# Optimization experiments

Hardware: AMD Instinct MI355X
Metric: run time of the kernel (lower is better)

## Reference

```python
import jax, jax.numpy as jnp
import numpy as np

B, N, E = 2, 2048, 1024
H, D = 16, 64


def setup_inputs() -> dict:
    key = jax.random.key(0)
    k1, k2, k3 = jax.random.split(key, 3)
    x = jax.random.normal(k1, (B, N, E), dtype=jnp.float32)
    Wqkv = jax.random.normal(k2, (3 * H * D, E), dtype=jnp.float32) * 0.02
    bqkv = jnp.zeros((3 * H * D,), dtype=jnp.float32)
    Wout = jax.random.normal(k3, (E, H * D), dtype=jnp.float32) * 0.02
    bout = jnp.zeros((E,), dtype=jnp.float32)
    return {"x": x, "Wqkv": Wqkv, "bqkv": bqkv, "Wout": Wout, "bout": bout}


def reference(x, Wqkv, bqkv, Wout, bout):
    b, n, _ = x.shape
    scale = D ** (-0.5)
    # qkv projection: [b, n, 3*h*d], interpreted as (h, d, qkv) per einops pattern
    qkv = (x @ Wqkv.T + bqkv).reshape(b, n, H, D, 3)
    q = jnp.transpose(qkv[..., 0], (0, 2, 1, 3))  # [b, h, n, d]
    k = jnp.transpose(qkv[..., 1], (0, 2, 1, 3))
    v = jnp.transpose(qkv[..., 2], (0, 2, 1, 3))
    att = jnp.einsum('bhid,bhjd->bhij', q, k) * scale  # [b, h, n, n]
    causal = jnp.tril(jnp.ones((n, n), dtype=bool))
    att = jnp.where(causal, att, -jnp.inf)
    att = jax.nn.softmax(att, axis=-1)
    out = jnp.einsum('bhij,bhjd->bhid', att, v)  # [b, h, n, d]
    out = jnp.transpose(out, (0, 2, 1, 3)).reshape(b, n, H * D)
    return out @ Wout.T + bout
```

## Files before the change

### kernel.cpp

```cpp
#include <hip/hip_runtime.h>
#include <hip/hip_bf16.h>

#define B_ 2
#define N_ 2048
#define E_ 1024
#define H_ 16
#define D_ 64
#define M_ 4096
#define HD_ 1024
#define NT_ 3072

using f32x4  = __attribute__((ext_vector_type(4))) float;
using f32x16 = __attribute__((ext_vector_type(16))) float;
using bf16x8 = __attribute__((ext_vector_type(8))) short;

static __device__ __forceinline__ unsigned short f2bf(float f) {
  union { float f; unsigned u; } v; v.f = f;
  unsigned r = v.u + 0x7FFF + ((v.u >> 16) & 1);
  return (unsigned short)(r >> 16);
}
static __device__ __forceinline__ float bf2f(short s) {
  union { unsigned u; float f; } v; v.u = ((unsigned)(unsigned short)s) << 16; return v.f;
}

static __device__ __forceinline__ void gld16(const void* g, void* l) {
  __builtin_amdgcn_global_load_lds(
      (const __attribute__((address_space(1))) unsigned int*)g,
      (__attribute__((address_space(3))) unsigned int*)l, 16, 0, 0);
}

static __device__ __forceinline__ unsigned cvtpk(float lo, float hi) {
  unsigned r;
  asm("v_cvt_pk_bf16_f32 %0, %1, %2" : "=v"(r) : "v"(lo), "v"(hi));
  return r;
}
static __device__ __forceinline__ void pl32swap(unsigned& a, unsigned& b) {
  asm("v_permlane32_swap_b32 %0, %1" : "+v"(a), "+v"(b));
}

static __device__ __forceinline__ int gswz(int row) {
  return ((row >> 1) & 3) ^ ((row >> 3) & 1);
}


__global__ void k_cvt_x(const float* __restrict__ x, unsigned short* __restrict__ xb) {
  int t = blockIdx.x * 256 + threadIdx.x;
  float4 v = reinterpret_cast<const float4*>(x)[t];
  ushort4 o;
  o.x = f2bf(v.x); o.y = f2bf(v.y); o.z = f2bf(v.z); o.w = f2bf(v.w);
  reinterpret_cast<ushort4*>(xb)[t] = o;
}

__global__ void k_cvt_wqkv(const float* __restrict__ w, const float* __restrict__ bsrc,
                           unsigned short* __restrict__ wb, float* __restrict__ br) {
  int t = blockIdx.x * 256 + threadIdx.x;
  int r = t >> 8;
  int c = (t & 255) * 4;
  int kind = r >> 10, hd = r & 1023;
  int h = hd >> 6, d = hd & 63;
  int rin = h * 192 + d * 3 + kind;
  float s = (kind == 0) ? 0.125f * 1.4426950408889634f : 1.0f;
  float4 v = *reinterpret_cast<const float4*>(w + (size_t)rin * E_ + c);
  ushort4 o;
  o.x = f2bf(v.x * s); o.y = f2bf(v.y * s); o.z = f2bf(v.z * s); o.w = f2bf(v.w * s);
  *reinterpret_cast<ushort4*>(wb + (size_t)r * E_ + c) = o;
  if (c == 0) br[r] = bsrc[rin] * s;
}

__global__ void k_cvt_wout(const float* __restrict__ w, unsigned short* __restrict__ wb) {
  int t = blockIdx.x * 256 + threadIdx.x;
  int r = t >> 8;
  int c = (t & 255) * 4;
  float4 v = *reinterpret_cast<const float4*>(w + (size_t)r * HD_ + c);
  ushort4 o;
  o.x = f2bf(v.x); o.y = f2bf(v.y); o.z = f2bf(v.z); o.w = f2bf(v.w);
  *reinterpret_cast<ushort4*>(wb + (size_t)r * HD_ + c) = o;
}

template <int EPI, int BM>
__global__ __launch_bounds__(256, 2) void k_gemm(
    const unsigned short* __restrict__ A,
    const unsigned short* __restrict__ W,
    const float* __restrict__ bias,
    unsigned short* __restrict__ Qo, unsigned short* __restrict__ Ko,
    unsigned short* __restrict__ Vo, float* __restrict__ Fo,
    int M, int Nt, int K)
{
  constexpr int APT = (BM == 128) ? 2 : 1;
  constexpr int LPI = APT + 2;
  constexpr int NF  = (BM == 128) ? 4 : 2;
  __shared__ unsigned short As[3][BM * 32];
  __shared__ unsigned short Bs[3][128 * 32];
  const int t = threadIdx.x;
  const int w = t >> 6, l = t & 63, lg = l >> 4, lr = l & 15;
  const int wrow0 = (BM == 128) ? (w >> 1) * 64 : 0;
  const int wcol0 = (BM == 128) ? (w & 1) * 64 : w * 32;
  const int row0 = blockIdx.x * BM, col0 = blockIdx.y * 128;
  const int NT = K >> 5;

  f32x4 acc[4][NF] = {};

  auto stage = [&](int b, int k0) {
#pragma unroll
    for (int c = 0; c < APT; ++c) {
      int ci = w * APT + c;
      int row = ci * 16 + (l >> 2);
      int sub = (l & 3) ^ gswz(row);
      gld16(A + (size_t)(row0 + row) * K + k0 + sub * 8,
            (unsigned short*)&As[b][0] + ci * 512);
    }
#pragma unroll
    for (int c = 0; c < 2; ++c) {
      int ci = w * 2 + c;
      int row = ci * 16 + (l >> 2);
      int sub = (l & 3) ^ gswz(row);
      gld16(W + (size_t)(col0 + row) * K + k0 + sub * 8,
            (unsigned short*)&Bs[b][0] + ci * 512);
    }
  };

  stage(0, 0);
  stage(1, 32);

  for (int kt = 0; kt < NT; ++kt) {
    const int ib = kt % 3;
    if (kt + 2 < NT) stage((kt + 2) % 3, (kt + 2) * 32);
    const int na = NT - 1 - kt;
    if (na >= 2) {
      if constexpr (LPI == 4) asm volatile("s_waitcnt vmcnt(8)" ::: "memory");
      else                    asm volatile("s_waitcnt vmcnt(6)" ::: "memory");
    } else if (na == 1) {
      if constexpr (LPI == 4) asm volatile("s_waitcnt vmcnt(4)" ::: "memory");
      else                    asm volatile("s_waitcnt vmcnt(3)" ::: "memory");
    } else {
      asm volatile("s_waitcnt vmcnt(0)" ::: "memory");
    }
    asm volatile("s_barrier" ::: "memory");

    bf16x8 af[4], bf[NF];
#pragma unroll
    for (int m = 0; m < 4; ++m) {
      int row = wrow0 + m * 16 + lr;
      af[m] = *reinterpret_cast<const bf16x8*>(
          &As[ib][row * 32 + ((lg ^ gswz(row)) * 8)]);
    }
#pragma unroll
    for (int n = 0; n < NF; ++n) {
      int row = wcol0 + n * 16 + lr;
      bf[n] = *reinterpret_cast<const bf16x8*>(
          &Bs[ib][row * 32 + ((lg ^ gswz(row)) * 8)]);
    }
    __builtin_amdgcn_s_setprio(1);
#pragma unroll
    for (int m = 0; m < 4; ++m)
#pragma unroll
      for (int n = 0; n < NF; ++n)
        acc[m][n] = __builtin_amdgcn_mfma_f32_16x16x32_bf16(af[m], bf[n], acc[m][n], 0, 0, 0);
    __builtin_amdgcn_s_setprio(0);

    asm volatile("s_barrier" ::: "memory");
  }

#pragma unroll
  for (int m = 0; m < 4; ++m) {
#pragma unroll
    for (int n = 0; n < NF; ++n) {
      int col = col0 + wcol0 + n * 16 + lr;
      float bb = bias[col];
#pragma unroll
      for (int rr = 0; rr < 4; ++rr) {
        int ro = row0 + wrow0 + m * 16 + lg * 4 + rr;
        float val = acc[m][n][rr] + bb;
        if (EPI == 0) {
          int kind = col >> 10, hd = col & 1023, h = hd >> 6, d = hd & 63;
          int bi = ro >> 11, ni = ro & 2047;
          unsigned short bv = f2bf(val);
          size_t bh = (size_t)(bi * H_ + h);
          if (kind == 0)      Qo[(bh * N_ + ni) * D_ + d] = bv;
          else if (kind == 1) Ko[(bh * N_ + ni) * D_ + d] = bv;
          else                Vo[bh * (size_t)(D_ * N_) + (size_t)d * N_ + ni] = bv;
        } else {
          Fo[(size_t)ro * HD_ + col] = val;
        }
      }
    }
  }
}

__global__ __launch_bounds__(256, 3) void k_attn(
    const unsigned short* __restrict__ Q,
    const unsigned short* __restrict__ Kg,
    const unsigned short* __restrict__ Vg,
    unsigned short* __restrict__ O,
    unsigned short* __restrict__ Pp,
    float* __restrict__ Pml)
{
  static const int u_qt[24] = {15,15,14,13,12,11,10, 9,   8, 7,14, 6,13, 5,12, 4,   8, 0, 9, 1,10, 2,11, 3};
  static const int u_t0[24] = { 0,16, 0, 0, 0, 0, 0, 0,   0, 0,16, 0,16, 0,16, 0,  16, 0,16, 0,16, 0,16, 0};
  static const int u_ps[24] = {14,15,12,10, 8, 6, 4, 2,   0,-1,13,-1,11,-1, 9,-1,   1,-1, 3,-1, 5,-1, 7,-1};

  __shared__ unsigned short Ks[3][64 * 64];
  __shared__ unsigned short Vs[3][64 * 64];

  const int t = threadIdx.x;
  const int w = t >> 6, l = t & 63;
  const int lq = l & 31;
  const int hi = l >> 5;
  const int bh = blockIdx.x & 31;
  const int u  = blockIdx.x >> 5;
  const int qt = u_qt[u], t0 = u_t0[u], ps = u_ps[u];
  const int q0 = qt * 128;
  const int r0w = q0 + w * 32;
  const int rtop = r0w + 31;
  const bool splitc0 = (ps >= 0) && (t0 == 0);
  const int tendW = splitc0 ? 16 : ((rtop >> 6) + 1);
  const int tendB = splitc0 ? 16 : (((q0 + 127) >> 6) + 1);

  const unsigned short* Qb = Q  + (size_t)bh * (N_ * D_);
  const unsigned short* Kb = Kg + (size_t)bh * (N_ * D_);
  const unsigned short* Vb = Vg + (size_t)bh * (N_ * D_);

  const int pr  = l >> 3;
  const int pswz = ((l & 7) ^ pr) * 8;
  const unsigned short* KsrcB = Kb + pr * D_ + pswz;
  const unsigned short* VsrcB = Vb + pr * N_ + pswz;

  bf16x8 qf[4];
#pragma unroll
  for (int ks = 0; ks < 4; ++ks)
    qf[ks] = *reinterpret_cast<const bf16x8*>(
        Qb + (size_t)(r0w + lq) * D_ + ks * 16 + hi * 8);

  f32x16 oacc[2] = {};
  float lrun = 0.f;

  auto stage = [&](int b, int kt_) {
    const int kv = kt_ * 64;
#pragma unroll
    for (int c = 0; c < 2; ++c) {
      int cb = w * 2 + c;
      gld16(KsrcB + kv * D_ + cb * 512, (unsigned short*)&Ks[b][0] + cb * 512);
      gld16(VsrcB + kv + cb * 8 * N_,   (unsigned short*)&Vs[b][0] + cb * 512);
    }
  };

  stage(0, t0);
  if (t0 + 1 < tendB) stage(1, t0 + 1);

  for (int kt = t0; kt < tendB; ++kt) {
    const int ib = (kt - t0) % 3;
    if (kt + 2 < tendB) stage((kt - t0 + 2) % 3, kt + 2);
    const int na = tendB - 1 - kt;
    if (na >= 2)      asm volatile("s_waitcnt vmcnt(8)" ::: "memory");
    else if (na == 1) asm volatile("s_waitcnt vmcnt(4)" ::: "memory");
    else              asm volatile("s_waitcnt vmcnt(0)" ::: "memory");
    asm volatile("s_barrier" ::: "memory");

    if (kt < tendW) {
      const int kv0 = kt * 64;
      bf16x8 kf[2][4], vf[2][4];
#pragma unroll
      for (int ct = 0; ct < 2; ++ct)
#pragma unroll
        for (int ks = 0; ks < 4; ++ks) {
          int row = ct * 32 + lq;
          kf[ct][ks] = *reinterpret_cast<const bf16x8*>(
              &Ks[ib][row * 64 + (((ks * 2 + hi) ^ (lq & 7)) * 8)]);
        }
#pragma unroll
      for (int dt = 0; dt < 2; ++dt)
#pragma unroll
        for (int j = 0; j < 4; ++j) {
          int row = dt * 32 + lq;
          vf[dt][j] = *reinterpret_cast<const bf16x8*>(
              &Vs[ib][row * 64 + (((j * 2 + hi) ^ (lq & 7)) * 8)]);
        }

      f32x16 sct[2];
      __builtin_amdgcn_s_setprio(1);
#pragma unroll
      for (int ct = 0; ct < 2; ++ct) {
        f32x16 z = {};
#pragma unroll
        for (int ks = 0; ks < 4; ++ks)
          z = __builtin_amdgcn_mfma_f32_32x32x16_bf16(kf[ct][ks], qf[ks], z, 0, 0, 0);
        sct[ct] = z;
      }
      __builtin_amdgcn_s_setprio(0);

      if (kv0 + 63 > r0w) {
        int qrow = r0w + lq;
#pragma unroll
        for (int ct = 0; ct < 2; ++ct)
#pragma unroll
          for (int r = 0; r < 16; ++r) {
            int kv = kv0 + ct * 32 + (r & 3) + 8 * (r >> 2) + 4 * hi;
            if (kv > qrow) sct[ct][r] = -1e30f;
          }
      }

      float s16[16];
#pragma unroll
      for (int r = 0; r < 16; ++r) {
        float p0 = exp2f(sct[0][r]);
        float p1 = exp2f(sct[1][r]);
        sct[0][r] = p0; sct[1][r] = p1;
        s16[r] = p0 + p1;
      }
#pragma unroll
      for (int st = 8; st >= 1; st >>= 1)
#pragma unroll
        for (int r = 0; r < 8; ++r)
          if (r < st) s16[r] += s16[r + st];
      lrun += s16[0] + __shfl_xor(s16[0], 32);

      bf16x8 paf[4];
#pragma unroll
      for (int ct = 0; ct < 2; ++ct) {
        unsigned u0 = cvtpk(sct[ct][0],  sct[ct][1]);
        unsigned u1 = cvtpk(sct[ct][2],  sct[ct][3]);
        unsigned u2 = cvtpk(sct[ct][4],  sct[ct][5]);
        unsigned u3 = cvtpk(sct[ct][6],  sct[ct][7]);
        unsigned u4 = cvtpk(sct[ct][8],  sct[ct][9]);
        unsigned u5 = cvtpk(sct[ct][10], sct[ct][11]);
        unsigned u6 = cvtpk(sct[ct][12], sct[ct][13]);
        unsigned u7 = cvtpk(sct[ct][14], sct[ct][15]);
        pl32swap(u0, u2); pl32swap(u1, u3);
        pl32swap(u4, u6); pl32swap(u5, u7);
        union { unsigned uu[4]; bf16x8 v; } c0, c1;
        c0.uu[0] = u0; c0.uu[1] = u1; c0.uu[2] = u2; c0.uu[3] = u3;
        c1.uu[0] = u4; c1.uu[1] = u5; c1.uu[2] = u6; c1.uu[3] = u7;
        paf[ct * 2]     = c0.v;
        paf[ct * 2 + 1] = c1.v;
      }

      __builtin_amdgcn_s_setprio(1);
#pragma unroll
      for (int dt = 0; dt < 2; ++dt)
#pragma unroll
        for (int j = 0; j < 4; ++j)
          oacc[dt] = __builtin_amdgcn_mfma_f32_32x32x16_bf16(paf[j], vf[dt][j], oacc[dt], 0, 0, 0);
      __builtin_amdgcn_s_setprio(0);
    }

    asm volatile("s_barrier" ::: "memory");
  }

  int bi = bh >> 4, h = bh & 15;
  if (ps < 0) {
    float inv = 1.0f / lrun;
    float iv[16];
#pragma unroll
    for (int r = 0; r < 16; ++r)
      iv[r] = __shfl(inv, (r & 3) + 8 * (r >> 2) + 4 * hi);
#pragma unroll
    for (int dt = 0; dt < 2; ++dt)
#pragma unroll
      for (int r = 0; r < 16; ++r) {
        int qr = r0w + (r & 3) + 8 * (r >> 2) + 4 * hi;
        int d = dt * 32 + lq;
        O[((size_t)(bi * N_ + qr) * H_ + h) * D_ + d] = f2bf(oacc[dt][r] * iv[r]);
      }
  } else {
    unsigned short* pb = Pp + (size_t)(bh * 16 + ps) * (128 * 64);
    float* mb = Pml + (size_t)(bh * 16 + ps) * 128;
#pragma unroll
    for (int dt = 0; dt < 2; ++dt)
#pragma unroll
      for (int r = 0; r < 16; ++r) {
        int rloc = w * 32 + (r & 3) + 8 * (r >> 2) + 4 * hi;
        pb[rloc * 64 + dt * 32 + lq] = f2bf(oacc[dt][r]);
      }
    if (l < 32) {
      int rloc = w * 32 + l;
      mb[rloc] = lrun;
    }
  }
}

__global__ void k_merge(const unsigned short* __restrict__ Pp,
                        const float* __restrict__ Pml,
                        unsigned short* __restrict__ O) {
  int t = blockIdx.x * 256 + threadIdx.x;
  int dseg = t & 7;
  int rloc = (t >> 3) & 127;
  int qt8 = (t >> 10) & 7;
  int bh  = t >> 13;
  size_t b0 = (size_t)(bh * 16 + qt8 * 2) * 128 + rloc;
  size_t b1 = b0 + 128;
  bf16x8 o0 = *reinterpret_cast<const bf16x8*>(Pp + b0 * 64 + dseg * 8);
  bf16x8 o1 = *reinterpret_cast<const bf16x8*>(Pp + b1 * 64 + dseg * 8);
  float l0 = Pml[b0], l1 = Pml[b1];
  float inv = 1.0f / (l0 + l1);
  int n = (qt8 + 8) * 128 + rloc;
  int bi = bh >> 4, h = bh & 15;
  unsigned short* op = O + ((size_t)(bi * N_ + n) * H_ + h) * D_ + dseg * 8;
  bf16x8 res;
#pragma unroll
  for (int j = 0; j < 8; ++j)
    res[j] = (short)f2bf((bf2f(o0[j]) + bf2f(o1[j])) * inv);
  *reinterpret_cast<bf16x8*>(op) = res;
}


extern "C" void kernel_launch(void* const* d_in, const int* in_sizes, int n_in,
                              void* d_out, int out_size, void* d_ws, size_t ws_size,
                              hipStream_t stream) {
  const float* x    = (const float*)d_in[0];
  const float* Wqkv = (const float*)d_in[1];
  const float* bqkv = (const float*)d_in[2];
  const float* Wout = (const float*)d_in[3];
  const float* bout = (const float*)d_in[4];
  float* out = (float*)d_out;

  char* ws = (char*)d_ws;
  unsigned short* xb  = (unsigned short*)ws; ws += (size_t)M_ * E_ * 2;
  unsigned short* wqb = (unsigned short*)ws; ws += (size_t)NT_ * E_ * 2;
  float*          bqr = (float*)ws;          ws += 16384;
  unsigned short* wob = (unsigned short*)ws; ws += (size_t)E_ * HD_ * 2;
  unsigned short* Qb  = (unsigned short*)ws; ws += (size_t)M_ * D_ * H_ * 2;
  unsigned short* Kb  = (unsigned short*)ws; ws += (size_t)M_ * D_ * H_ * 2;
  unsigned short* Vb  = (unsigned short*)ws; ws += (size_t)M_ * D_ * H_ * 2;
  unsigned short* ao  = (unsigned short*)ws; ws += (size_t)M_ * HD_ * 2;

  unsigned short* Pp  = xb;
  float*          Pml = (float*)wqb;

  k_cvt_x<<<(M_ * E_) / 4 / 256, 256, 0, stream>>>(x, xb);
  k_cvt_wqkv<<<NT_, 256, 0, stream>>>(Wqkv, bqkv, wqb, bqr);
  k_cvt_wout<<<E_, 256, 0, stream>>>(Wout, wob);

  k_gemm<0, 128><<<dim3(M_ / 128, NT_ / 128), 256, 0, stream>>>(
      xb, wqb, bqr, Qb, Kb, Vb, nullptr, M_, NT_, E_);

  k_attn<<<768, 256, 0, stream>>>(Qb, Kb, Vb, ao, Pp, Pml);
  k_merge<<<1024, 256, 0, stream>>>(Pp, Pml, ao);

  k_gemm<1, 64><<<dim3(M_ / 64, HD_ / 128), 256, 0, stream>>>(
      ao, wob, bout, nullptr, nullptr, nullptr, out, M_, HD_, E_);
}
```

Measured before the change: 118.5 us.

## Double-step GEMM k-loop with 4-stage buffers and transpose V separately

```diff
diff --git a/kernel.cpp b/kernel.cpp
--- a/kernel.cpp
+++ b/kernel.cpp
@@ -77,6 +77,32 @@
   *reinterpret_cast<ushort4*>(wb + (size_t)r * HD_ + c) = o;
 }
 
+__global__ void k_vt(const unsigned short* __restrict__ Vr,
+                     unsigned short* __restrict__ Vt) {
+  __shared__ unsigned short tile[64][68];
+  int bh = blockIdx.x & 31;
+  int nt = blockIdx.x >> 5;
+  int t = threadIdx.x;
+  int r = t >> 3, c8 = (t & 7) * 8;
+#pragma unroll
+  for (int h = 0; h < 2; ++h) {
+    bf16x8 v = *reinterpret_cast<const bf16x8*>(
+        Vr + ((size_t)bh * N_ + nt * 64 + r + h * 32) * D_ + c8);
+#pragma unroll
+    for (int j = 0; j < 8; ++j) tile[r + h * 32][c8 + j] = (unsigned short)v[j];
+  }
+  __syncthreads();
+#pragma unroll
+  for (int h = 0; h < 2; ++h) {
+    int d = (t >> 3) + h * 32;
+    int n0 = (t & 7) * 8;
+    bf16x8 o;
+#pragma unroll
+    for (int j = 0; j < 8; ++j) o[j] = (short)tile[n0 + j][d];
+    *reinterpret_cast<bf16x8*>(Vt + ((size_t)bh * D_ + d) * N_ + nt * 64 + n0) = o;
+  }
+}
+
 template <int EPI, int BM>
 __global__ __launch_bounds__(256, 2) void k_gemm(
     const unsigned short* __restrict__ A,
@@ -89,8 +115,8 @@
   constexpr int APT = (BM == 128) ? 2 : 1;
   constexpr int LPI = APT + 2;
   constexpr int NF  = (BM == 128) ? 4 : 2;
-  __shared__ unsigned short As[3][BM * 32];
-  __shared__ unsigned short Bs[3][128 * 32];
+  __shared__ unsigned short As[4][BM * 32];
+  __shared__ unsigned short Bs[4][128 * 32];
   const int t = threadIdx.x;
   const int w = t >> 6, l = t & 63, lg = l >> 4, lr = l & 15;
   const int wrow0 = (BM == 128) ? (w >> 1) * 64 : 0;
@@ -119,24 +145,7 @@
     }
   };
 
-  stage(0, 0);
-  stage(1, 32);
-
-  for (int kt = 0; kt < NT; ++kt) {
-    const int ib = kt % 3;
-    if (kt + 2 < NT) stage((kt + 2) % 3, (kt + 2) * 32);
-    const int na = NT - 1 - kt;
-    if (na >= 2) {
-      if constexpr (LPI == 4) asm volatile("s_waitcnt vmcnt(8)" ::: "memory");
-      else                    asm volatile("s_waitcnt vmcnt(6)" ::: "memory");
-    } else if (na == 1) {
-      if constexpr (LPI == 4) asm volatile("s_waitcnt vmcnt(4)" ::: "memory");
-      else                    asm volatile("s_waitcnt vmcnt(3)" ::: "memory");
-    } else {
-      asm volatile("s_waitcnt vmcnt(0)" ::: "memory");
-    }
-    asm volatile("s_barrier" ::: "memory");
-
+  auto compute = [&](int ib) {
     bf16x8 af[4], bf[NF];
 #pragma unroll
     for (int m = 0; m < 4; ++m) {
@@ -157,7 +166,24 @@
       for (int n = 0; n < NF; ++n)
         acc[m][n] = __builtin_amdgcn_mfma_f32_16x16x32_bf16(af[m], bf[n], acc[m][n], 0, 0, 0);
     __builtin_amdgcn_s_setprio(0);
-
+  };
+
+  stage(0, 0);
+  stage(1, 32);
+  const int NP = NT >> 1;
+  for (int p = 0; p < NP; ++p) {
+    const int t0 = 2 * p;
+    if (t0 + 2 < NT) {
+      stage((t0 + 2) & 3, (t0 + 2) * 32);
+      stage((t0 + 3) & 3, (t0 + 3) * 32);
+      if constexpr (LPI == 4) asm volatile("s_waitcnt vmcnt(8)" ::: "memory");
+      else                    asm volatile("s_waitcnt vmcnt(6)" ::: "memory");
+    } else {
+      asm volatile("s_waitcnt vmcnt(0)" ::: "memory");
+    }
+    asm volatile("s_barrier" ::: "memory");
+    compute(t0 & 3);
+    compute((t0 + 1) & 3);
     asm volatile("s_barrier" ::: "memory");
   }
 
@@ -178,7 +204,7 @@
           size_t bh = (size_t)(bi * H_ + h);
           if (kind == 0)      Qo[(bh * N_ + ni) * D_ + d] = bv;
           else if (kind == 1) Ko[(bh * N_ + ni) * D_ + d] = bv;
-          else                Vo[bh * (size_t)(D_ * N_) + (size_t)d * N_ + ni] = bv;
+          else                Vo[(bh * N_ + ni) * D_ + d] = bv;
         } else {
           Fo[(size_t)ro * HD_ + col] = val;
         }
@@ -423,6 +449,7 @@
   unsigned short* Vb  = (unsigned short*)ws; ws += (size_t)M_ * D_ * H_ * 2;
   unsigned short* ao  = (unsigned short*)ws; ws += (size_t)M_ * HD_ * 2;
 
+  unsigned short* Vraw = ao;
   unsigned short* Pp  = xb;
   float*          Pml = (float*)wqb;
 
@@ -431,7 +458,9 @@
   k_cvt_wout<<<E_, 256, 0, stream>>>(Wout, wob);
 
   k_gemm<0, 128><<<dim3(M_ / 128, NT_ / 128), 256, 0, stream>>>(
-      xb, wqb, bqr, Qb, Kb, Vb, nullptr, M_, NT_, E_);
+      xb, wqb, bqr, Qb, Kb, Vraw, nullptr, M_, NT_, E_);
+
+  k_vt<<<1024, 256, 0, stream>>>(Vraw, Vb);
 
   k_attn<<<768, 256, 0, stream>>>(Qb, Kb, Vb, ao, Pp, Pml);
   k_merge<<<1024, 256, 0, stream>>>(Pp, Pml, ao);
```

Result: no change. 119.1 us (+0.5%).

## Software-pipeline QK^T of the next KV tile ahead of the current softmax

Applied to the files above, without the earlier changes.

```diff
diff --git a/kernel.cpp b/kernel.cpp
--- a/kernel.cpp
+++ b/kernel.cpp
@@ -244,50 +244,61 @@
     }
   };
 
+  auto read_kf = [&](int b, bf16x8 kf[2][4]) {
+#pragma unroll
+    for (int ct = 0; ct < 2; ++ct)
+#pragma unroll
+      for (int ks = 0; ks < 4; ++ks) {
+        int row = ct * 32 + lq;
+        kf[ct][ks] = *reinterpret_cast<const bf16x8*>(
+            &Ks[b][row * 64 + (((ks * 2 + hi) ^ (lq & 7)) * 8)]);
+      }
+  };
+
   stage(0, t0);
-  if (t0 + 1 < tendB) stage(1, t0 + 1);
+  stage(1, t0 + 1);
+  asm volatile("s_waitcnt vmcnt(4)" ::: "memory");
+  __syncthreads();
+
+  f32x16 scur[2];
+  {
+    bf16x8 kf[2][4];
+    read_kf(0, kf);
+#pragma unroll
+    for (int ct = 0; ct < 2; ++ct) {
+      f32x16 z = {};
+#pragma unroll
+      for (int ks = 0; ks < 4; ++ks)
+        z = __builtin_amdgcn_mfma_f32_32x32x16_bf16(kf[ct][ks], qf[ks], z, 0, 0, 0);
+      scur[ct] = z;
+    }
+  }
 
   for (int kt = t0; kt < tendB; ++kt) {
-    const int ib = (kt - t0) % 3;
-    if (kt + 2 < tendB) stage((kt - t0 + 2) % 3, kt + 2);
-    const int na = tendB - 1 - kt;
-    if (na >= 2)      asm volatile("s_waitcnt vmcnt(8)" ::: "memory");
-    else if (na == 1) asm volatile("s_waitcnt vmcnt(4)" ::: "memory");
-    else              asm volatile("s_waitcnt vmcnt(0)" ::: "memory");
+    const int ib  = (kt - t0) % 3;
+    const int ib1 = (kt - t0 + 1) % 3;
+    if (kt + 2 < tendB) {
+      stage((kt - t0 + 2) % 3, kt + 2);
+      asm volatile("s_waitcnt vmcnt(4)" ::: "memory");
+    } else {
+      asm volatile("s_waitcnt vmcnt(0)" ::: "memory");
+    }
     asm volatile("s_barrier" ::: "memory");
+
+    bf16x8 kf[2][4];
+    read_kf(ib1, kf);
+    f32x16 snext[2];
+#pragma unroll
+    for (int ct = 0; ct < 2; ++ct) {
+      f32x16 z = {};
+#pragma unroll
+      for (int ks = 0; ks < 4; ++ks)
+        z = __builtin_amdgcn_mfma_f32_32x32x16_bf16(kf[ct][ks], qf[ks], z, 0, 0, 0);
+      snext[ct] = z;
+    }
 
     if (kt < tendW) {
       const int kv0 = kt * 64;
-      bf16x8 kf[2][4], vf[2][4];
-#pragma unroll
-      for (int ct = 0; ct < 2; ++ct)
-#pragma unroll
-        for (int ks = 0; ks < 4; ++ks) {
-          int row = ct * 32 + lq;
-          kf[ct][ks] = *reinterpret_cast<const bf16x8*>(
-              &Ks[ib][row * 64 + (((ks * 2 + hi) ^ (lq & 7)) * 8)]);
-        }
-#pragma unroll
-      for (int dt = 0; dt < 2; ++dt)
-#pragma unroll
-        for (int j = 0; j < 4; ++j) {
-          int row = dt * 32 + lq;
-          vf[dt][j] = *reinterpret_cast<const bf16x8*>(
-              &Vs[ib][row * 64 + (((j * 2 + hi) ^ (lq & 7)) * 8)]);
-        }
-
-      f32x16 sct[2];
-      __builtin_amdgcn_s_setprio(1);
-#pragma unroll
-      for (int ct = 0; ct < 2; ++ct) {
-        f32x16 z = {};
-#pragma unroll
-        for (int ks = 0; ks < 4; ++ks)
-          z = __builtin_amdgcn_mfma_f32_32x32x16_bf16(kf[ct][ks], qf[ks], z, 0, 0, 0);
-        sct[ct] = z;
-      }
-      __builtin_amdgcn_s_setprio(0);
-
       if (kv0 + 63 > r0w) {
         int qrow = r0w + lq;
 #pragma unroll
@@ -295,16 +306,16 @@
 #pragma unroll
           for (int r = 0; r < 16; ++r) {
             int kv = kv0 + ct * 32 + (r & 3) + 8 * (r >> 2) + 4 * hi;
-            if (kv > qrow) sct[ct][r] = -1e30f;
+            if (kv > qrow) scur[ct][r] = -1e30f;
           }
       }
 
       float s16[16];
 #pragma unroll
       for (int r = 0; r < 16; ++r) {
-        float p0 = exp2f(sct[0][r]);
-        float p1 = exp2f(sct[1][r]);
-        sct[0][r] = p0; sct[1][r] = p1;
+        float p0 = exp2f(scur[0][r]);
+        float p1 = exp2f(scur[1][r]);
+        scur[0][r] = p0; scur[1][r] = p1;
         s16[r] = p0 + p1;
       }
 #pragma unroll
@@ -317,14 +328,14 @@
       bf16x8 paf[4];
 #pragma unroll
       for (int ct = 0; ct < 2; ++ct) {
-        unsigned u0 = cvtpk(sct[ct][0],  sct[ct][1]);
-        unsigned u1 = cvtpk(sct[ct][2],  sct[ct][3]);
-        unsigned u2 = cvtpk(sct[ct][4],  sct[ct][5]);
-        unsigned u3 = cvtpk(sct[ct][6],  sct[ct][7]);
-        unsigned u4 = cvtpk(sct[ct][8],  sct[ct][9]);
-        unsigned u5 = cvtpk(sct[ct][10], sct[ct][11]);
-        unsigned u6 = cvtpk(sct[ct][12], sct[ct][13]);
-        unsigned u7 = cvtpk(sct[ct][14], sct[ct][15]);
+        unsigned u0 = cvtpk(scur[ct][0],  scur[ct][1]);
+        unsigned u1 = cvtpk(scur[ct][2],  scur[ct][3]);
+        unsigned u2 = cvtpk(scur[ct][4],  scur[ct][5]);
+        unsigned u3 = cvtpk(scur[ct][6],  scur[ct][7]);
+        unsigned u4 = cvtpk(scur[ct][8],  scur[ct][9]);
+        unsigned u5 = cvtpk(scur[ct][10], scur[ct][11]);
+        unsigned u6 = cvtpk(scur[ct][12], scur[ct][13]);
+        unsigned u7 = cvtpk(scur[ct][14], scur[ct][15]);
         pl32swap(u0, u2); pl32swap(u1, u3);
         pl32swap(u4, u6); pl32swap(u5, u7);
         union { unsigned uu[4]; bf16x8 v; } c0, c1;
@@ -334,6 +345,15 @@
         paf[ct * 2 + 1] = c1.v;
       }
 
+      bf16x8 vf[2][4];
+#pragma unroll
+      for (int dt = 0; dt < 2; ++dt)
+#pragma unroll
+        for (int j = 0; j < 4; ++j) {
+          int row = dt * 32 + lq;
+          vf[dt][j] = *reinterpret_cast<const bf16x8*>(
+              &Vs[ib][row * 64 + (((j * 2 + hi) ^ (lq & 7)) * 8)]);
+        }
       __builtin_amdgcn_s_setprio(1);
 #pragma unroll
       for (int dt = 0; dt < 2; ++dt)
@@ -343,6 +363,8 @@
       __builtin_amdgcn_s_setprio(0);
     }
 
+    scur[0] = snext[0];
+    scur[1] = snext[1];
     asm volatile("s_barrier" ::: "memory");
   }
 
```

New measurement: 118.2 us. About the same (-0.2%).
